# Kernel tuning notes

Hardware: AMD Instinct MI355X
Metric: run time of the kernel (lower is better)

Reference implementation:

```python
import jax, jax.numpy as jnp
import numpy as np

N_NODES = 50000
N_EDGES = 800000
D_IN, D_HID, N_CLS, N_PROT = 128, 256, 16, 512
EPS = 1e-6


def setup_inputs() -> dict:
    key = jax.random.key(0)
    ks = jax.random.split(key, 12)
    s = 0.05
    return {
        "x": jax.random.normal(ks[0], (N_NODES, D_IN), dtype=jnp.float32),
        "edge_index": jax.random.randint(ks[1], (2, N_EDGES), 0, N_NODES, dtype=jnp.int64),
        "prot": jax.random.randint(ks[2], (N_PROT,), 0, N_NODES, dtype=jnp.int64),
        "epoch": 1,
        "W0": jax.random.normal(ks[3], (D_IN, D_HID), dtype=jnp.float32) * s,
        "b0": jnp.zeros((D_HID,), jnp.float32),
        "W1": jax.random.normal(ks[4], (D_HID, D_HID), dtype=jnp.float32) * s,
        "b1": jnp.zeros((D_HID,), jnp.float32),
        "Wl1": jax.random.normal(ks[5], (D_HID, D_HID), dtype=jnp.float32) * s,
        "bl1": jnp.zeros((D_HID,), jnp.float32),
        "Wl2": jax.random.normal(ks[6], (D_HID, N_CLS), dtype=jnp.float32) * s,
        "bl2": jnp.zeros((N_CLS,), jnp.float32),
    }


def _gcn_layer(h, W, b, src, dst, norm, n):
    # PyG GCNConv: h' = scatter_add(norm * (h @ W)[src] -> dst) + b
    m = (h @ W)[src] * norm[:, None]
    return jax.ops.segment_sum(m, dst, num_segments=n) + b


def _forward(x, edge_index, prot, W0, b0, W1, b1, Wl1, bl1, Wl2, bl2):
    n = x.shape[0]
    loops = jnp.arange(n, dtype=edge_index.dtype)
    src = jnp.concatenate([edge_index[0], loops])
    dst = jnp.concatenate([edge_index[1], loops])
    deg = jax.ops.segment_sum(jnp.ones_like(dst, dtype=x.dtype), dst, num_segments=n)
    dis = jax.lax.rsqrt(deg)  # deg >= 1 thanks to self loops
    norm = dis[src] * dis[dst]

    h = jax.nn.relu(_gcn_layer(x, W0, b0, src, dst, norm, n))
    h = _gcn_layer(h, W1, b1, src, dst, norm, n)

    # L2 row-normalize (torch divides by the norm directly)
    qn = jnp.linalg.norm(h, axis=1, keepdims=True)
    h = h / qn

    # relative_rep: cosine similarity of every node to each anchor
    anchors = h[prot]                             # [P, H]
    nx = jnp.linalg.norm(h, axis=1)               # [N]
    na = jnp.linalg.norm(anchors, axis=1)         # [P]
    num = h @ anchors.T                           # [N, P]
    x_rel = num / jnp.maximum(nx[:, None] * na[None, :], EPS)

    # classifier head on prototypes -> out_proto, then composed prediction
    lin = lambda z: jax.nn.relu(z @ Wl1 + bl1) @ Wl2 + bl2
    out_proto = jax.nn.log_softmax(lin(anchors), axis=-1)   # [P, C]
    out = jax.nn.log_softmax(x_rel @ out_proto, axis=-1)    # [N, C]
    return out, x_rel, out_proto


def reference(x, edge_index, prot, epoch, W0, b0, W1, b1, Wl1, bl1, Wl2, bl2):
    # epoch >= first_step_epochs (=0) branch: inference-path composition
    return _forward(x, edge_index, prot, W0, b0, W1, b1, Wl1, bl1, Wl2, bl2)


if __name__ == "__main__":
    out, x_rel, out_proto = reference(**setup_inputs())
    print(out.shape, x_rel.shape, out_proto.shape)
```

## Files before the change

### kernel.cpp

```cpp
#include <hip/hip_runtime.h>
#include <hip/hip_bf16.h>
#include <math.h>

#define NN 50000
#define NP 50048
#define EE 800000
#define DIN 128
#define HID 256
#define NCLS 16
#define NPROT 512

typedef __attribute__((ext_vector_type(8))) short short8;
typedef __attribute__((ext_vector_type(4))) float f32x4;

__device__ inline unsigned short f2b(float f) {
    union { float f; unsigned u; } c; c.f = f;
    unsigned u = c.u;
    unsigned r = (u + 0x7FFFu + ((u >> 16) & 1u)) >> 16;
    return (unsigned short)r;
}
__device__ inline float b2f(unsigned short u) {
    union { unsigned u; float f; } c; c.u = ((unsigned)u) << 16; return c.f;
}

#define GL2LDS16(g, l)                                                              \
    __builtin_amdgcn_global_load_lds(                                               \
        (const __attribute__((address_space(1))) unsigned int*)(g),                 \
        (__attribute__((address_space(3))) unsigned int*)(l), 16, 0, 0)


__global__ __launch_bounds__(256) void k_count(const int* __restrict__ dst, int* __restrict__ cnt, int e) {
    int i = blockIdx.x * 256 + threadIdx.x;
    if (i < e) atomicAdd(&cnt[dst[i]], 1);
}

__global__ __launch_bounds__(256) void k_scan1(const int* __restrict__ cnt, int* __restrict__ excl,
                                               int* __restrict__ bsum, float* __restrict__ dis, int n) {
    __shared__ int s[256];
    int t = threadIdx.x;
    int i = blockIdx.x * 256 + t;
    int v = (i < n) ? cnt[i] : 0;
    if (i < n) dis[i] = rsqrtf((float)v + 1.0f);
    s[t] = v; __syncthreads();
    for (int d = 1; d < 256; d <<= 1) {
        int add = (t >= d) ? s[t - d] : 0;
        __syncthreads();
        s[t] += add;
        __syncthreads();
    }
    if (i < n) excl[i] = s[t] - v;
    if (t == 255) bsum[blockIdx.x] = s[255];
}

__global__ __launch_bounds__(256) void k_scan2(const int* __restrict__ bsum, int* __restrict__ boff, int nb) {
    __shared__ int s[256];
    int t = threadIdx.x;
    int v = (t < nb) ? bsum[t] : 0;
    s[t] = v; __syncthreads();
    for (int d = 1; d < 256; d <<= 1) {
        int add = (t >= d) ? s[t - d] : 0;
        __syncthreads();
        s[t] += add;
        __syncthreads();
    }
    if (t < nb) boff[t] = s[t] - v;
}

__global__ __launch_bounds__(256) void k_scan3(const int* __restrict__ excl, const int* __restrict__ boff,
                                               int* __restrict__ off, int n, int e) {
    int i = blockIdx.x * 256 + threadIdx.x;
    if (i < n) off[i] = excl[i] + boff[blockIdx.x];
    if (i == 0) off[n] = e;
}

__global__ __launch_bounds__(256) void k_fill(const int* __restrict__ src, const int* __restrict__ dst,
                                              const int* __restrict__ off, int* __restrict__ cursor,
                                              const float* __restrict__ dis,
                                              int2* __restrict__ csr_e, int e) {
    int i = blockIdx.x * 256 + threadIdx.x;
    if (i >= e) return;
    int s = src[i], d = dst[i];
    int pos = atomicAdd(&cursor[d], 1);
    csr_e[off[d] + pos] = make_int2(s, __float_as_int(dis[s] * dis[d]));
}


#define CAST_BLKS (NN * DIN / 4 / 256)
#define WT0_BLKS  (DIN * HID / 256)
#define WT1_BLKS  (HID * HID / 256)

__global__ __launch_bounds__(256) void k_prep(const float* __restrict__ x, unsigned short* __restrict__ xb,
                                              const float* __restrict__ W0, unsigned short* __restrict__ Wt0,
                                              const float* __restrict__ W1, unsigned short* __restrict__ Wt1) {
    int b = blockIdx.x, t = threadIdx.x;
    if (b < CAST_BLKS) {
        int i = b * 256 + t;
        float4 v = ((const float4*)x)[i];
        ushort4 o; o.x = f2b(v.x); o.y = f2b(v.y); o.z = f2b(v.z); o.w = f2b(v.w);
        ((ushort4*)xb)[i] = o;
    } else if (b < CAST_BLKS + WT0_BLKS) {
        int i = (b - CAST_BLKS) * 256 + t;
        int k = i / HID, n = i - k * HID;
        Wt0[n * DIN + k] = f2b(W0[(size_t)k * HID + n]);
    } else {
        int i = (b - CAST_BLKS - WT0_BLKS) * 256 + t;
        int k = i / HID, n = i - k * HID;
        Wt1[n * HID + k] = f2b(W1[(size_t)k * HID + n]);
    }
}


__global__ __launch_bounds__(256) void k_gemm_mfma(const unsigned short* __restrict__ A,
                                                   const unsigned short* __restrict__ Bt,
                                                   void* __restrict__ C, int M, int Nc, int K, int mode,
                                                   const float* __restrict__ bias) {
    __shared__ __align__(16) unsigned short As[128 * 32];
    __shared__ __align__(16) unsigned short Bs[128 * 32];
    const int t = threadIdx.x;
    const int lane = t & 63;
    const int quad = lane >> 4;
    const int l16 = lane & 15;
    const int wv = t >> 6;
    const int wm = (wv & 1) * 64, wn = (wv >> 1) * 64;
    const int m0 = blockIdx.y * 128, n0 = blockIdx.x * 128;

    f32x4 acc[4][4];
#pragma unroll
    for (int i = 0; i < 4; ++i)
#pragma unroll
        for (int j = 0; j < 4; ++j)
#pragma unroll
            for (int r = 0; r < 4; ++r) acc[i][j][r] = 0.0f;

    const int sr = t >> 2;
    const int sc = (t & 3) * 8;

    for (int k0 = 0; k0 < K; k0 += 32) {
        GL2LDS16(A + (size_t)(m0 + sr) * K + k0 + sc,       &As[t * 8]);
        GL2LDS16(A + (size_t)(m0 + 64 + sr) * K + k0 + sc,  &As[2048 + t * 8]);
        GL2LDS16(Bt + (size_t)(n0 + sr) * K + k0 + sc,      &Bs[t * 8]);
        GL2LDS16(Bt + (size_t)(n0 + 64 + sr) * K + k0 + sc, &Bs[2048 + t * 8]);
        __syncthreads();
        short8 af[4], bf[4];
#pragma unroll
        for (int i = 0; i < 4; ++i)
            af[i] = *(const short8*)&As[(wm + i * 16 + l16) * 32 + quad * 8];
#pragma unroll
        for (int j = 0; j < 4; ++j)
            bf[j] = *(const short8*)&Bs[(wn + j * 16 + l16) * 32 + quad * 8];
#pragma unroll
        for (int i = 0; i < 4; ++i)
#pragma unroll
            for (int j = 0; j < 4; ++j)
                acc[i][j] = __builtin_amdgcn_mfma_f32_16x16x32_bf16(af[i], bf[j], acc[i][j], 0, 0, 0);
        __syncthreads();
    }

#pragma unroll
    for (int i = 0; i < 4; ++i) {
        int rb = m0 + wm + i * 16 + quad * 4;
#pragma unroll
        for (int j = 0; j < 4; ++j) {
            int col = n0 + wn + j * 16 + l16;
#pragma unroll
            for (int rg = 0; rg < 4; ++rg) {
                int r = rb + rg;
                float v = acc[i][j][rg];
                if (mode == 0) {
                    ((unsigned short*)C)[(size_t)r * Nc + col] = f2b(v);
                } else {
                    v = fmaxf(v + bias[col], 0.0f);
                    ((unsigned short*)C)[(size_t)r * Nc + col] = f2b(v);
                }
            }
        }
    }
}


__global__ __launch_bounds__(256) void k_agg128(const unsigned short* __restrict__ xw, const int* __restrict__ off,
                                                const int2* __restrict__ csr, const float* __restrict__ dis,
                                                unsigned short* __restrict__ out, int n) {
    int node = (blockIdx.x * 256 + threadIdx.x) >> 6;
    int lane = threadIdx.x & 63;
    if (node >= n) return;
    float d = dis[node];
    float w0 = d * d;
    ushort2 u = ((const ushort2*)(xw + (size_t)node * DIN))[lane];
    float a0 = w0 * b2f(u.x), a1 = w0 * b2f(u.y);
    int p = off[node], p1 = off[node + 1];
#define G128(e)                                                           \
    {                                                                     \
        ushort2 v = ((const ushort2*)(xw + (size_t)(e).x * DIN))[lane];   \
        float w = __int_as_float((e).y);                                  \
        a0 = fmaf(w, b2f(v.x), a0); a1 = fmaf(w, b2f(v.y), a1);           \
    }
    for (; p + 3 < p1; p += 4) {
        int2 e0 = csr[p], e1 = csr[p + 1], e2 = csr[p + 2], e3 = csr[p + 3];
        G128(e0) G128(e1) G128(e2) G128(e3)
    }
    for (; p < p1; ++p) { int2 e0 = csr[p]; G128(e0) }
#undef G128
    ushort2 o; o.x = f2b(a0); o.y = f2b(a1);
    ((ushort2*)(out + (size_t)node * DIN))[lane] = o;
}


__global__ __launch_bounds__(256) void k_agg256(const unsigned short* __restrict__ xw, const int* __restrict__ off,
                                                const int2* __restrict__ csr, const float* __restrict__ dis,
                                                const float* __restrict__ bias,
                                                unsigned short* __restrict__ out, float* __restrict__ nx, int n) {
    int node = (blockIdx.x * 256 + threadIdx.x) >> 6;
    int lane = threadIdx.x & 63;
    if (node >= n) return;
    float d = dis[node];
    float w0 = d * d;
    ushort4 u = ((const ushort4*)(xw + (size_t)node * HID))[lane];
    float a0 = w0 * b2f(u.x), a1 = w0 * b2f(u.y), a2 = w0 * b2f(u.z), a3 = w0 * b2f(u.w);
    int p = off[node], p1 = off[node + 1];
#define G256(e)                                                           \
    {                                                                     \
        ushort4 v = ((const ushort4*)(xw + (size_t)(e).x * HID))[lane];   \
        float w = __int_as_float((e).y);                                  \
        a0 = fmaf(w, b2f(v.x), a0); a1 = fmaf(w, b2f(v.y), a1);           \
        a2 = fmaf(w, b2f(v.z), a2); a3 = fmaf(w, b2f(v.w), a3);           \
    }
    for (; p + 3 < p1; p += 4) {
        int2 e0 = csr[p], e1 = csr[p + 1], e2 = csr[p + 2], e3 = csr[p + 3];
        G256(e0) G256(e1) G256(e2) G256(e3)
    }
    for (; p < p1; ++p) { int2 e0 = csr[p]; G256(e0) }
#undef G256
    float4 b = ((const float4*)bias)[lane];
    a0 += b.x; a1 += b.y; a2 += b.z; a3 += b.w;
    float ss = a0 * a0 + a1 * a1 + a2 * a2 + a3 * a3;
    for (int m = 32; m >= 1; m >>= 1) ss += __shfl_xor(ss, m, 64);
    float qn = sqrtf(ss);
    a0 /= qn; a1 /= qn; a2 /= qn; a3 /= qn;
    float s2 = a0 * a0 + a1 * a1 + a2 * a2 + a3 * a3;
    for (int m = 32; m >= 1; m >>= 1) s2 += __shfl_xor(s2, m, 64);
    if (lane == 0) nx[node] = sqrtf(s2);
    ushort4 o; o.x = f2b(a0); o.y = f2b(a1); o.z = f2b(a2); o.w = f2b(a3);
    ((ushort4*)(out + (size_t)node * HID))[lane] = o;
}


__global__ __launch_bounds__(256) void k_gproto(const unsigned short* __restrict__ hb,
                                                const int* __restrict__ prot, const float* __restrict__ nx,
                                                unsigned short* __restrict__ aRb, float* __restrict__ na,
                                                const float* __restrict__ Wl1, const float* __restrict__ bl1,
                                                const float* __restrict__ Wl2, const float* __restrict__ bl2,
                                                float* __restrict__ outp) {
    __shared__ float sa[HID];
    __shared__ float st[HID];
    int row = blockIdx.x, t = threadIdx.x;
    int p = prot[row];
    unsigned short us = hb[(size_t)p * HID + t];
    aRb[(size_t)row * HID + t] = us;
    sa[t] = b2f(us);
    if (t == 0) na[row] = nx[p];
    __syncthreads();
    float acc = bl1[t];
#pragma unroll 8
    for (int k = 0; k < HID; ++k) acc = fmaf(sa[k], Wl1[k * HID + t], acc);
    st[t] = fmaxf(acc, 0.0f);
    __syncthreads();
    if (t < 64) {
        int c = t & 15, ch = t >> 4;
        float z = 0.f;
#pragma unroll 8
        for (int k = ch * 64; k < ch * 64 + 64; ++k) z = fmaf(st[k], Wl2[k * NCLS + c], z);
        z += __shfl_xor(z, 16, 64);
        z += __shfl_xor(z, 32, 64);
        z += bl2[c];
        float m = z;
        for (int d = 8; d >= 1; d >>= 1) m = fmaxf(m, __shfl_xor(m, d, 64));
        float e = expf(z - m);
        float s = e;
        for (int d = 8; d >= 1; d >>= 1) s += __shfl_xor(s, d, 64);
        if (t < 16) outp[row * NCLS + c] = z - m - logf(s);
    }
}


#define XST 136

__global__ __launch_bounds__(256) void k_xrel_out(const unsigned short* __restrict__ A,
                                                  const unsigned short* __restrict__ Bt,
                                                  const float* __restrict__ nx, const float* __restrict__ na,
                                                  const float* __restrict__ proto,
                                                  float* __restrict__ xrel, float* __restrict__ out) {
    __shared__ __align__(16) unsigned short As[128 * 32];
    __shared__ __align__(16) unsigned short Bs[128 * 32];
    __shared__ __align__(16) unsigned short Xs[128 * XST];
    __shared__ __align__(16) unsigned short pTc[16 * XST];

    const int t = threadIdx.x;
    const int lane = t & 63;
    const int quad = lane >> 4;
    const int l16 = lane & 15;
    const int wv = t >> 6;
    const int wm = (wv & 1) * 64, wn = (wv >> 1) * 64;
    const int m0 = blockIdx.x * 128;

    float nxv[4][4];
#pragma unroll
    for (int i = 0; i < 4; ++i)
#pragma unroll
        for (int rg = 0; rg < 4; ++rg) {
            int r = m0 + wm + i * 16 + quad * 4 + rg;
            nxv[i][rg] = nx[r < NN ? r : NN - 1];
        }

    const int sr = t >> 2;
    const int sc = (t & 3) * 8;

    f32x4 oacc[2];
#pragma unroll
    for (int r = 0; r < 4; ++r) { oacc[0][r] = 0.0f; oacc[1][r] = 0.0f; }

    for (int n0 = 0; n0 < NPROT; n0 += 128) {
        f32x4 acc[4][4];
#pragma unroll
        for (int i = 0; i < 4; ++i)
#pragma unroll
            for (int j = 0; j < 4; ++j)
#pragma unroll
                for (int r = 0; r < 4; ++r) acc[i][j][r] = 0.0f;

        for (int k0 = 0; k0 < HID; k0 += 32) {
            GL2LDS16(A + (size_t)(m0 + sr) * HID + k0 + sc,       &As[t * 8]);
            GL2LDS16(A + (size_t)(m0 + 64 + sr) * HID + k0 + sc,  &As[2048 + t * 8]);
            GL2LDS16(Bt + (size_t)(n0 + sr) * HID + k0 + sc,      &Bs[t * 8]);
            GL2LDS16(Bt + (size_t)(n0 + 64 + sr) * HID + k0 + sc, &Bs[2048 + t * 8]);
            __syncthreads();
            short8 af[4], bf[4];
#pragma unroll
            for (int i = 0; i < 4; ++i)
                af[i] = *(const short8*)&As[(wm + i * 16 + l16) * 32 + quad * 8];
#pragma unroll
            for (int j = 0; j < 4; ++j)
                bf[j] = *(const short8*)&Bs[(wn + j * 16 + l16) * 32 + quad * 8];
#pragma unroll
            for (int i = 0; i < 4; ++i)
#pragma unroll
                for (int j = 0; j < 4; ++j)
                    acc[i][j] = __builtin_amdgcn_mfma_f32_16x16x32_bf16(af[i], bf[j], acc[i][j], 0, 0, 0);
            __syncthreads();
        }

        for (int i = t; i < 128 * NCLS; i += 256) {
            int kk = i >> 4, c = i & 15;
            pTc[c * XST + kk] = f2b(proto[(n0 + kk) * NCLS + c]);
        }

        float nav[4];
#pragma unroll
        for (int j = 0; j < 4; ++j) nav[j] = na[n0 + wn + j * 16 + l16];
#pragma unroll
        for (int i = 0; i < 4; ++i) {
            int rls = (wm + i * 16 + quad * 4) * XST;
#pragma unroll
            for (int j = 0; j < 4; ++j) {
                int cl = wn + j * 16 + l16;
#pragma unroll
                for (int rg = 0; rg < 4; ++rg) {
                    float s = fmaxf(nxv[i][rg] * nav[j], 1e-6f);
                    float v = acc[i][j][rg] * __builtin_amdgcn_rcpf(s);
                    Xs[rls + rg * XST + cl] = f2b(v);
                }
            }
        }
        __syncthreads();

#pragma unroll
        for (int ii = 0; ii < 2; ++ii) {
            int rb = wv * 32 + ii * 16;
#pragma unroll
            for (int ks = 0; ks < 4; ++ks) {
                short8 af = *(const short8*)&Xs[(rb + l16) * XST + ks * 32 + quad * 8];
                short8 pb = *(const short8*)&pTc[l16 * XST + ks * 32 + quad * 8];
                oacc[ii] = __builtin_amdgcn_mfma_f32_16x16x32_bf16(af, pb, oacc[ii], 0, 0, 0);
            }
        }

#pragma unroll
        for (int it = 0; it < 8; ++it) {
            int idx = it * 256 + t;
            int row = idx >> 4;
            int c8 = (idx & 15) * 8;
            int r = m0 + row;
            if (r < NN) {
                short8 u = *(const short8*)&Xs[row * XST + c8];
                float* dst = &xrel[(size_t)r * NPROT + n0 + c8];
                float4 v0, v1;
                v0.x = b2f((unsigned short)u[0]); v0.y = b2f((unsigned short)u[1]);
                v0.z = b2f((unsigned short)u[2]); v0.w = b2f((unsigned short)u[3]);
                v1.x = b2f((unsigned short)u[4]); v1.y = b2f((unsigned short)u[5]);
                v1.z = b2f((unsigned short)u[6]); v1.w = b2f((unsigned short)u[7]);
                *(float4*)dst = v0;
                *(float4*)(dst + 4) = v1;
            }
        }
    }

#pragma unroll
    for (int ii = 0; ii < 2; ++ii) {
#pragma unroll
        for (int rg = 0; rg < 4; ++rg) {
            int row = m0 + wv * 32 + ii * 16 + quad * 4 + rg;
            float z = oacc[ii][rg];
            float mx = z;
            for (int d = 8; d >= 1; d >>= 1) mx = fmaxf(mx, __shfl_xor(mx, d, 64));
            float e = expf(z - mx);
            float ssum = e;
            for (int d = 8; d >= 1; d >>= 1) ssum += __shfl_xor(ssum, d, 64);
            if (row < NN) out[(size_t)row * NCLS + l16] = z - mx - logf(ssum);
        }
    }
}


extern "C" void kernel_launch(void* const* d_in, const int* in_sizes, int n_in,
                              void* d_out, int out_size, void* d_ws, size_t ws_size,
                              hipStream_t stream) {
    const float* x    = (const float*)d_in[0];
    const int*   eidx = (const int*)d_in[1];
    const int*   prot = (const int*)d_in[2];
    const float* W0  = (const float*)d_in[4];
    const float* b0  = (const float*)d_in[5];
    const float* W1  = (const float*)d_in[6];
    const float* b1  = (const float*)d_in[7];
    const float* Wl1 = (const float*)d_in[8];
    const float* bl1 = (const float*)d_in[9];
    const float* Wl2 = (const float*)d_in[10];
    const float* bl2 = (const float*)d_in[11];

    const int N = NN, E = EE;
    const int* esrc_in = eidx;
    const int* edst_in = eidx + E;

    float* out_final = (float*)d_out;
    float* x_rel     = (float*)d_out + (size_t)N * NCLS;
    float* out_proto = x_rel + (size_t)N * NPROT;

    char* w = (char*)d_ws;
    auto alloc = [&](size_t bytes) { char* p = w; w += (bytes + 255) & ~(size_t)255; return p; };
    int*   cnt      = (int*)alloc((size_t)N * 4);
    int*   cursor   = (int*)alloc((size_t)N * 4);
    float* dis      = (float*)alloc((size_t)N * 4);
    int*   excl     = (int*)alloc((size_t)N * 4);
    int*   csr_off  = (int*)alloc((size_t)(N + 1) * 4);
    int*   bsum     = (int*)alloc(1024);
    int*   boff     = (int*)alloc(1024);
    int2*  csr_e    = (int2*)alloc((size_t)E * 8);
    float* nx       = (float*)alloc((size_t)N * 4);
    float* na       = (float*)alloc((size_t)NPROT * 4);
    unsigned short* xb    = (unsigned short*)alloc((size_t)NP * DIN * 2);
    unsigned short* Wt0   = (unsigned short*)alloc((size_t)HID * DIN * 2);
    unsigned short* Wt1   = (unsigned short*)alloc((size_t)HID * HID * 2);
    unsigned short* bufAb = (unsigned short*)alloc((size_t)NP * HID * 2);
    unsigned short* h0b   = (unsigned short*)alloc((size_t)NP * HID * 2);
    unsigned short* aRb   = (unsigned short*)alloc((size_t)NPROT * HID * 2);
    unsigned short* a1 = bufAb;
    unsigned short* hb = h0b;

    hipMemsetAsync(cnt, 0, (size_t)N * 4, stream);
    hipMemsetAsync(cursor, 0, (size_t)N * 4, stream);

    k_count<<<(E + 255) / 256, 256, 0, stream>>>(edst_in, cnt, E);
    int NB = (N + 255) / 256;
    k_scan1<<<NB, 256, 0, stream>>>(cnt, excl, bsum, dis, N);
    k_scan2<<<1, 256, 0, stream>>>(bsum, boff, NB);
    k_scan3<<<NB, 256, 0, stream>>>(excl, boff, csr_off, N, E);
    k_fill<<<(E + 255) / 256, 256, 0, stream>>>(esrc_in, edst_in, csr_off, cursor, dis, csr_e, E);

    k_prep<<<CAST_BLKS + WT0_BLKS + WT1_BLKS, 256, 0, stream>>>(x, xb, W0, Wt0, W1, Wt1);

    const int MT = NP / 128;

    k_agg128<<<(N + 3) / 4, 256, 0, stream>>>(xb, csr_off, csr_e, dis, a1, N);
    k_gemm_mfma<<<dim3(HID / 128, MT), 256, 0, stream>>>(a1, Wt0, h0b, N, HID, DIN, 2, b0);

    k_gemm_mfma<<<dim3(HID / 128, MT), 256, 0, stream>>>(h0b, Wt1, bufAb, N, HID, HID, 0, nullptr);
    k_agg256<<<(N + 3) / 4, 256, 0, stream>>>(bufAb, csr_off, csr_e, dis, b1, hb, nx, N);

    k_gproto<<<NPROT, 256, 0, stream>>>(hb, prot, nx, aRb, na, Wl1, bl1, Wl2, bl2, out_proto);

    k_xrel_out<<<MT, 256, 0, stream>>>(hb, aRb, nx, na, out_proto, x_rel, out_final);
}
```

Baseline: 479.4 us.

## Split xrel kernel across prototype chunks with partial-sum reduce kernel

The x_rel/out kernel previously looped over four 128-prototype chunks inside one block per 128 rows, giving only about 391 blocks. Each block now handles one (row tile, prototype chunk) pair, so there are four times as many blocks. Block IDs are remapped so that blocks sharing a row tile land on the same XCD, the Xs staging buffer uses an XOR swizzle instead of padding, and launch bounds request 3 blocks per CU. The partial logits are written to a workspace and summed by a new reduction kernel that applies the log_softmax. This trades an extra launch and a round trip through global memory for the partials in exchange for higher occupancy and better parallelism.

```diff
diff --git a/kernel.cpp b/kernel.cpp
--- a/kernel.cpp
+++ b/kernel.cpp
@@ -283,17 +283,26 @@
 }
 
 
-#define XST 136
-
-__global__ __launch_bounds__(256) void k_xrel_out(const unsigned short* __restrict__ A,
-                                                  const unsigned short* __restrict__ Bt,
-                                                  const float* __restrict__ nx, const float* __restrict__ na,
-                                                  const float* __restrict__ proto,
-                                                  float* __restrict__ xrel, float* __restrict__ out) {
+#define XSW(row, cs) (((cs) ^ (((row) & 7) << 3)))
+#define NWGX (4 * (NP / 128))
+
+__global__ __launch_bounds__(256, 3) void k_xrel_out(const unsigned short* __restrict__ A,
+                                                     const unsigned short* __restrict__ Bt,
+                                                     const float* __restrict__ nx, const float* __restrict__ na,
+                                                     const float* __restrict__ proto,
+                                                     float* __restrict__ xrel, float* __restrict__ opart) {
     __shared__ __align__(16) unsigned short As[128 * 32];
     __shared__ __align__(16) unsigned short Bs[128 * 32];
-    __shared__ __align__(16) unsigned short Xs[128 * XST];
-    __shared__ __align__(16) unsigned short pTc[16 * XST];
+    __shared__ __align__(16) unsigned short Xs[128 * 128];
+    __shared__ __align__(16) unsigned short pTc[16 * 136];
+
+    const int bid = blockIdx.x;
+    const int q = NWGX / 8, r = NWGX % 8;
+    const int xcd = bid & 7, li = bid >> 3;
+    const int wk = (xcd < r ? xcd * (q + 1) : r * (q + 1) + (xcd - r) * q) + li;
+    const int m0 = (wk >> 2) * 128;
+    const int nc = wk & 3;
+    const int n0 = nc * 128;
 
     const int t = threadIdx.x;
     const int lane = t & 63;
@@ -301,123 +310,126 @@
     const int l16 = lane & 15;
     const int wv = t >> 6;
     const int wm = (wv & 1) * 64, wn = (wv >> 1) * 64;
-    const int m0 = blockIdx.x * 128;
 
     float nxv[4][4];
 #pragma unroll
     for (int i = 0; i < 4; ++i)
 #pragma unroll
         for (int rg = 0; rg < 4; ++rg) {
-            int r = m0 + wm + i * 16 + quad * 4 + rg;
-            nxv[i][rg] = nx[r < NN ? r : NN - 1];
+            int rr = m0 + wm + i * 16 + quad * 4 + rg;
+            nxv[i][rg] = nx[rr < NN ? rr : NN - 1];
         }
+    float nav[4];
+#pragma unroll
+    for (int j = 0; j < 4; ++j) nav[j] = na[n0 + wn + j * 16 + l16];
 
     const int sr = t >> 2;
     const int sc = (t & 3) * 8;
 
-    f32x4 oacc[2];
-#pragma unroll
-    for (int r = 0; r < 4; ++r) { oacc[0][r] = 0.0f; oacc[1][r] = 0.0f; }
-
-    for (int n0 = 0; n0 < NPROT; n0 += 128) {
-        f32x4 acc[4][4];
+    f32x4 acc[4][4];
+#pragma unroll
+    for (int i = 0; i < 4; ++i)
+#pragma unroll
+        for (int j = 0; j < 4; ++j)
+#pragma unroll
+            for (int rr = 0; rr < 4; ++rr) acc[i][j][rr] = 0.0f;
+
+    for (int k0 = 0; k0 < HID; k0 += 32) {
+        GL2LDS16(A + (size_t)(m0 + sr) * HID + k0 + sc,       &As[t * 8]);
+        GL2LDS16(A + (size_t)(m0 + 64 + sr) * HID + k0 + sc,  &As[2048 + t * 8]);
+        GL2LDS16(Bt + (size_t)(n0 + sr) * HID + k0 + sc,      &Bs[t * 8]);
+        GL2LDS16(Bt + (size_t)(n0 + 64 + sr) * HID + k0 + sc, &Bs[2048 + t * 8]);
+        __syncthreads();
+        short8 af[4], bf[4];
 #pragma unroll
         for (int i = 0; i < 4; ++i)
+            af[i] = *(const short8*)&As[(wm + i * 16 + l16) * 32 + quad * 8];
+#pragma unroll
+        for (int j = 0; j < 4; ++j)
+            bf[j] = *(const short8*)&Bs[(wn + j * 16 + l16) * 32 + quad * 8];
+#pragma unroll
+        for (int i = 0; i < 4; ++i)
 #pragma unroll
             for (int j = 0; j < 4; ++j)
-#pragma unroll
-                for (int r = 0; r < 4; ++r) acc[i][j][r] = 0.0f;
-
-        for (int k0 = 0; k0 < HID; k0 += 32) {
-            GL2LDS16(A + (size_t)(m0 + sr) * HID + k0 + sc,       &As[t * 8]);
-            GL2LDS16(A + (size_t)(m0 + 64 + sr) * HID + k0 + sc,  &As[2048 + t * 8]);
-            GL2LDS16(Bt + (size_t)(n0 + sr) * HID + k0 + sc,      &Bs[t * 8]);
-            GL2LDS16(Bt + (size_t)(n0 + 64 + sr) * HID + k0 + sc, &Bs[2048 + t * 8]);
-            __syncthreads();
-            short8 af[4], bf[4];
-#pragma unroll
-            for (int i = 0; i < 4; ++i)
-                af[i] = *(const short8*)&As[(wm + i * 16 + l16) * 32 + quad * 8];
-#pragma unroll
-            for (int j = 0; j < 4; ++j)
-                bf[j] = *(const short8*)&Bs[(wn + j * 16 + l16) * 32 + quad * 8];
-#pragma unroll
-            for (int i = 0; i < 4; ++i)
-#pragma unroll
-                for (int j = 0; j < 4; ++j)
-                    acc[i][j] = __builtin_amdgcn_mfma_f32_16x16x32_bf16(af[i], bf[j], acc[i][j], 0, 0, 0);
-            __syncthreads();
-        }
-
-        for (int i = t; i < 128 * NCLS; i += 256) {
-            int kk = i >> 4, c = i & 15;
-            pTc[c * XST + kk] = f2b(proto[(n0 + kk) * NCLS + c]);
-        }
-
-        float nav[4];
-#pragma unroll
-        for (int j = 0; j < 4; ++j) nav[j] = na[n0 + wn + j * 16 + l16];
-#pragma unroll
-        for (int i = 0; i < 4; ++i) {
-            int rls = (wm + i * 16 + quad * 4) * XST;
-#pragma unroll
-            for (int j = 0; j < 4; ++j) {
-                int cl = wn + j * 16 + l16;
-#pragma unroll
-                for (int rg = 0; rg < 4; ++rg) {
-                    float s = fmaxf(nxv[i][rg] * nav[j], 1e-6f);
-                    float v = acc[i][j][rg] * __builtin_amdgcn_rcpf(s);
-                    Xs[rls + rg * XST + cl] = f2b(v);
-                }
+                acc[i][j] = __builtin_amdgcn_mfma_f32_16x16x32_bf16(af[i], bf[j], acc[i][j], 0, 0, 0);
+        __syncthreads();
+    }
+
+    for (int i = t; i < 128 * NCLS; i += 256) {
+        int kk = i >> 4, c = i & 15;
+        pTc[c * 136 + kk] = f2b(proto[(n0 + kk) * NCLS + c]);
+    }
+
+#pragma unroll
+    for (int i = 0; i < 4; ++i) {
+#pragma unroll
+        for (int j = 0; j < 4; ++j) {
+            int cl = wn + j * 16 + l16;
+#pragma unroll
+            for (int rg = 0; rg < 4; ++rg) {
+                int row = wm + i * 16 + quad * 4 + rg;
+                float s = fmaxf(nxv[i][rg] * nav[j], 1e-6f);
+                float v = acc[i][j][rg] * __builtin_amdgcn_rcpf(s);
+                Xs[row * 128 + XSW(row, cl)] = f2b(v);
             }
         }
-        __syncthreads();
-
-#pragma unroll
-        for (int ii = 0; ii < 2; ++ii) {
-            int rb = wv * 32 + ii * 16;
-#pragma unroll
-            for (int ks = 0; ks < 4; ++ks) {
-                short8 af = *(const short8*)&Xs[(rb + l16) * XST + ks * 32 + quad * 8];
-                short8 pb = *(const short8*)&pTc[l16 * XST + ks * 32 + quad * 8];
-                oacc[ii] = __builtin_amdgcn_mfma_f32_16x16x32_bf16(af, pb, oacc[ii], 0, 0, 0);
-            }
+    }
+    __syncthreads();
+
+    f32x4 oacc[2];
+#pragma unroll
+    for (int rr = 0; rr < 4; ++rr) { oacc[0][rr] = 0.0f; oacc[1][rr] = 0.0f; }
+#pragma unroll
+    for (int ii = 0; ii < 2; ++ii) {
+        int rb = wv * 32 + ii * 16;
+#pragma unroll
+        for (int ks = 0; ks < 4; ++ks) {
+            int row = rb + l16;
+            short8 af = *(const short8*)&Xs[row * 128 + XSW(row, ks * 32 + quad * 8)];
+            short8 pb = *(const short8*)&pTc[l16 * 136 + ks * 32 + quad * 8];
+            oacc[ii] = __builtin_amdgcn_mfma_f32_16x16x32_bf16(af, pb, oacc[ii], 0, 0, 0);
         }
-
-#pragma unroll
-        for (int it = 0; it < 8; ++it) {
-            int idx = it * 256 + t;
-            int row = idx >> 4;
-            int c8 = (idx & 15) * 8;
-            int r = m0 + row;
-            if (r < NN) {
-                short8 u = *(const short8*)&Xs[row * XST + c8];
-                float* dst = &xrel[(size_t)r * NPROT + n0 + c8];
-                float4 v0, v1;
-                v0.x = b2f((unsigned short)u[0]); v0.y = b2f((unsigned short)u[1]);
-                v0.z = b2f((unsigned short)u[2]); v0.w = b2f((unsigned short)u[3]);
-                v1.x = b2f((unsigned short)u[4]); v1.y = b2f((unsigned short)u[5]);
-                v1.z = b2f((unsigned short)u[6]); v1.w = b2f((unsigned short)u[7]);
-                *(float4*)dst = v0;
-                *(float4*)(dst + 4) = v1;
-            }
+    }
+#pragma unroll
+    for (int ii = 0; ii < 2; ++ii)
+#pragma unroll
+        for (int rg = 0; rg < 4; ++rg) {
+            int lrow = wv * 32 + ii * 16 + quad * 4 + rg;
+            opart[((size_t)nc * NP + m0 + lrow) * NCLS + l16] = oacc[ii][rg];
         }
-    }
-
-#pragma unroll
-    for (int ii = 0; ii < 2; ++ii) {
-#pragma unroll
-        for (int rg = 0; rg < 4; ++rg) {
-            int row = m0 + wv * 32 + ii * 16 + quad * 4 + rg;
-            float z = oacc[ii][rg];
-            float mx = z;
-            for (int d = 8; d >= 1; d >>= 1) mx = fmaxf(mx, __shfl_xor(mx, d, 64));
-            float e = expf(z - mx);
-            float ssum = e;
-            for (int d = 8; d >= 1; d >>= 1) ssum += __shfl_xor(ssum, d, 64);
-            if (row < NN) out[(size_t)row * NCLS + l16] = z - mx - logf(ssum);
+
+#pragma unroll
+    for (int it = 0; it < 8; ++it) {
+        int idx = it * 256 + t;
+        int row = idx >> 4;
+        int c8 = (idx & 15) * 8;
+        int rr = m0 + row;
+        if (rr < NN) {
+            short8 u = *(const short8*)&Xs[row * 128 + XSW(row, c8)];
+            float* dst = &xrel[(size_t)rr * NPROT + n0 + c8];
+            float4 v0, v1;
+            v0.x = b2f((unsigned short)u[0]); v0.y = b2f((unsigned short)u[1]);
+            v0.z = b2f((unsigned short)u[2]); v0.w = b2f((unsigned short)u[3]);
+            v1.x = b2f((unsigned short)u[4]); v1.y = b2f((unsigned short)u[5]);
+            v1.z = b2f((unsigned short)u[6]); v1.w = b2f((unsigned short)u[7]);
+            *(float4*)dst = v0;
+            *(float4*)(dst + 4) = v1;
         }
     }
+}
+
+
+__global__ __launch_bounds__(256) void k_reduce(const float* __restrict__ opart, float* __restrict__ out) {
+    int i = blockIdx.x * 256 + threadIdx.x;
+    int row = i >> 4, c = i & 15;
+    float z = opart[i] + opart[(size_t)NP * NCLS + i] + opart[(size_t)2 * NP * NCLS + i] +
+              opart[(size_t)3 * NP * NCLS + i];
+    float mx = z;
+    for (int d = 8; d >= 1; d >>= 1) mx = fmaxf(mx, __shfl_xor(mx, d, 64));
+    float e = expf(z - mx);
+    float s = e;
+    for (int d = 8; d >= 1; d >>= 1) s += __shfl_xor(s, d, 64);
+    if (row < NN) out[(size_t)row * NCLS + c] = z - mx - logf(s);
 }
 
 
@@ -456,6 +468,7 @@
     int2*  csr_e    = (int2*)alloc((size_t)E * 8);
     float* nx       = (float*)alloc((size_t)N * 4);
     float* na       = (float*)alloc((size_t)NPROT * 4);
+    float* opart    = (float*)alloc((size_t)4 * NP * NCLS * 4);
     unsigned short* xb    = (unsigned short*)alloc((size_t)NP * DIN * 2);
     unsigned short* Wt0   = (unsigned short*)alloc((size_t)HID * DIN * 2);
     unsigned short* Wt1   = (unsigned short*)alloc((size_t)HID * HID * 2);
@@ -487,5 +500,7 @@
 
     k_gproto<<<NPROT, 256, 0, stream>>>(hb, prot, nx, aRb, na, Wl1, bl1, Wl2, bl2, out_proto);
 
-    k_xrel_out<<<MT, 256, 0, stream>>>(hb, aRb, nx, na, out_proto, x_rel, out_final);
-}
+    k_xrel_out<<<NWGX, 256, 0, stream>>>(hb, aRb, nx, na, out_proto, x_rel, opart);
+
+    k_reduce<<<NP * NCLS / 256, 256, 0, stream>>>(opart, out_final);
+}
```

After: 447.1 us. 1.07x faster.
